# Kernel optimization log

Hardware: AMD Instinct MI355X
Metric: run time of the kernel (lower is better)

The kernel has to match this reference:

```python
import jax, jax.numpy as jnp
import numpy as np

N_NODES = 100000
N_EDGES = 1600000
IN_DIM = 48
HID = 16
N_CLASSES = 8


def _sage_conv(x, src, dst, W_l, W_r, b, n_nodes):
    # PyG SAGEConv (aggr='mean', root_weight=True):
    #   out_i = W_l @ mean_{j in N(i)} x_j + b + W_r @ x_i
    msg = x[src]                                              # [E, F]
    agg = jax.ops.segment_sum(msg, dst, num_segments=n_nodes)  # [N, F]
    deg = jax.ops.segment_sum(jnp.ones((src.shape[0],), x.dtype), dst,
                              num_segments=n_nodes)            # [N]
    agg = agg / jnp.maximum(deg, 1.0)[:, None]
    return agg @ W_l.T + b + x @ W_r.T


def setup_inputs() -> dict:
    key = jax.random.key(0)
    ks = jax.random.split(key, 10)
    def lin(k, out_d, in_d):
        s = 1.0 / np.sqrt(in_d)
        return jax.random.uniform(k, (out_d, in_d), jnp.float32, -s, s)
    x = jax.random.normal(ks[0], (N_NODES, IN_DIM), jnp.float32)
    edge_index = jax.random.randint(ks[1], (2, N_EDGES), 0, N_NODES, jnp.int64)
    return {
        "x": x,
        "edge_index": edge_index,
        "W1_l": lin(ks[2], HID, IN_DIM), "W1_r": lin(ks[3], HID, IN_DIM),
        "b1": jnp.zeros((HID,), jnp.float32),
        "W2_l": lin(ks[4], HID, HID), "W2_r": lin(ks[5], HID, HID),
        "b2": jnp.zeros((HID,), jnp.float32),
        "W3_l": lin(ks[6], N_CLASSES, HID), "W3_r": lin(ks[7], N_CLASSES, HID),
        "b3": jnp.zeros((N_CLASSES,), jnp.float32),
    }


def reference(x, edge_index, W1_l, W1_r, b1, W2_l, W2_r, b2, W3_l, W3_r, b3):
    src, dst = edge_index[0], edge_index[1]
    n = x.shape[0]
    # dropout is identity in deterministic/eval reference
    h = jax.nn.elu(_sage_conv(x, src, dst, W1_l, W1_r, b1, n))
    h = jax.nn.elu(_sage_conv(h, src, dst, W2_l, W2_r, b2, n))
    h = jax.nn.elu(_sage_conv(h, src, dst, W3_l, W3_r, b3, n))
    return jax.nn.log_softmax(h, axis=-1)
```

## Files before the change

kernel.cpp:

```cpp
#include <hip/hip_runtime.h>
#include <hip/hip_bf16.h>
#include <math.h>

#define N_IN   48
#define N_HID  16
#define N_CLS  8
#define CAP    48
#define NB_SHIFT 9
#define TILE   4096
#define CAPB   9216
#define WSTR   52

__device__ __forceinline__ float bf2f(unsigned short u) {
    union { unsigned int i; float f; } c;
    c.i = ((unsigned int)u) << 16;
    return c.f;
}
__device__ __forceinline__ unsigned short f2bf(float f) {
    unsigned int u = __float_as_uint(f);
    unsigned int r = u + 0x7FFFu + ((u >> 16) & 1u);
    return (unsigned short)(r >> 16);
}

__global__ __launch_bounds__(256) void proj48_kernel(
        const float* __restrict__ X,
        const float* __restrict__ Wl,
        const float* __restrict__ Wr,
        const float* __restrict__ b,
        unsigned short* __restrict__ P,
        float* __restrict__ S,
        int N) {
    __shared__ float sWl[N_HID * WSTR];
    __shared__ float sWr[N_HID * WSTR];
    __shared__ float sb[N_HID];
    int t = threadIdx.x;
    for (int idx = t; idx < N_HID * N_IN; idx += 256) {
        int r = idx / N_IN, k = idx - r * N_IN;
        sWl[r * WSTR + k] = Wl[idx];
        sWr[r * WSTR + k] = Wr[idx];
    }
    if (t < N_HID) sb[t] = b[t];
    __syncthreads();

    int node = blockIdx.x * 64 + (t >> 2);
    int q = t & 3;
    if (node >= N) return;

    const float4* xrow = reinterpret_cast<const float4*>(X + (size_t)node * N_IN);
    float accL[4], accR[4];
#pragma unroll
    for (int oo = 0; oo < 4; oo++) { accL[oo] = 0.0f; accR[oo] = sb[4 * q + oo]; }

#pragma unroll
    for (int c = 0; c < N_IN / 4; c++) {
        float4 xv = xrow[c];
#pragma unroll
        for (int oo = 0; oo < 4; oo++) {
            int row = 4 * q + oo;
            float4 wl = *reinterpret_cast<const float4*>(&sWl[row * WSTR + 4 * c]);
            float4 wr = *reinterpret_cast<const float4*>(&sWr[row * WSTR + 4 * c]);
            accL[oo] = fmaf(xv.x, wl.x, accL[oo]); accR[oo] = fmaf(xv.x, wr.x, accR[oo]);
            accL[oo] = fmaf(xv.y, wl.y, accL[oo]); accR[oo] = fmaf(xv.y, wr.y, accR[oo]);
            accL[oo] = fmaf(xv.z, wl.z, accL[oo]); accR[oo] = fmaf(xv.z, wr.z, accR[oo]);
            accL[oo] = fmaf(xv.w, wl.w, accL[oo]); accR[oo] = fmaf(xv.w, wr.w, accR[oo]);
        }
    }

    int gid = node * 4 + q;
    reinterpret_cast<ushort4*>(P)[gid] =
        make_ushort4(f2bf(accL[0]), f2bf(accL[1]), f2bf(accL[2]), f2bf(accL[3]));
    reinterpret_cast<float4*>(S)[gid] =
        make_float4(accR[0], accR[1], accR[2], accR[3]);
}

__global__ __launch_bounds__(256) void scatter_tiles_kernel(
        const int* __restrict__ src, const int* __restrict__ dst,
        int* __restrict__ cursor, int* __restrict__ ebuf, int E) {
    __shared__ int lh[256];
    __shared__ int gbase[256];
    __shared__ int rank[256];
    int t = threadIdx.x;
    lh[t] = 0;
    rank[t] = 0;
    __syncthreads();
    int base = blockIdx.x * TILE;
    int dcache[TILE / 256];
#pragma unroll
    for (int k = 0; k < TILE / 256; k++) {
        int e = base + t + k * 256;
        dcache[k] = -1;
        if (e < E) {
            int d = dst[e];
            dcache[k] = d;
            atomicAdd(&lh[d >> NB_SHIFT], 1);
        }
    }
    __syncthreads();
    if (lh[t]) gbase[t] = atomicAdd(&cursor[t], lh[t]);
    __syncthreads();
#pragma unroll
    for (int k = 0; k < TILE / 256; k++) {
        int e = base + t + k * 256;
        if (e < E) {
            int d = dcache[k];
            int b = d >> NB_SHIFT;
            int r = gbase[b] + atomicAdd(&rank[b], 1);
            if (r < CAPB)
                ebuf[b * CAPB + r] = ((d & 511) << 17) | src[e];
        }
    }
}

__global__ __launch_bounds__(256) void fine_fill_kernel(
        const int* __restrict__ cursor, const int* __restrict__ ebuf,
        int* __restrict__ cnt, int* __restrict__ adj, int N) {
    __shared__ int lc[512];
    int b = blockIdx.x;
    int nodeBeg = b << NB_SHIFT;
    for (int i = threadIdx.x; i < 512; i += 256) lc[i] = 0;
    __syncthreads();
    int beg = b * CAPB;
    int nb_cnt = cursor[b];
    if (nb_cnt > CAPB) nb_cnt = CAPB;
    int end = beg + nb_cnt;
    for (int e = beg + threadIdx.x; e < end; e += 256) {
        int v = ebuf[e];
        int ld = ((unsigned int)v) >> 17;
        int s  = v & 0x1FFFF;
        int p = atomicAdd(&lc[ld], 1);
        if (p < CAP) adj[(size_t)(nodeBeg + ld) * CAP + p] = s;
    }
    __syncthreads();
    for (int i = threadIdx.x; nodeBeg + i < N && i < 512; i += 256)
        cnt[nodeBeg + i] = lc[i];
}

__global__ __launch_bounds__(256) void gather_proj16_kernel(
        const int* __restrict__ cnt, const int* __restrict__ adj,
        const unsigned short* __restrict__ Pin, const float* __restrict__ Sin,
        const float* __restrict__ Wl, const float* __restrict__ Wr,
        const float* __restrict__ bias,
        unsigned short* __restrict__ Pout, float* __restrict__ Sout, int N) {
    int gid = blockIdx.x * blockDim.x + threadIdx.x;
    if (gid >= N * 4) return;
    int i = gid >> 2;
    int q = gid & 3;
    int deg = cnt[i];
    if (deg > CAP) deg = CAP;
    const int* lst = adj + (size_t)i * CAP;
    float4 sv = reinterpret_cast<const float4*>(Sin)[gid];
    float4 acc = make_float4(0.f, 0.f, 0.f, 0.f);
    const ushort4* P4 = reinterpret_cast<const ushort4*>(Pin);
    int e = 0;
    for (; e + 8 <= deg; e += 8) {
        int4 ja = *reinterpret_cast<const int4*>(lst + e);
        int4 jb = *reinterpret_cast<const int4*>(lst + e + 4);
        ushort4 t0 = P4[(size_t)ja.x * 4 + q];
        ushort4 t1 = P4[(size_t)ja.y * 4 + q];
        ushort4 t2 = P4[(size_t)ja.z * 4 + q];
        ushort4 t3 = P4[(size_t)ja.w * 4 + q];
        ushort4 t4 = P4[(size_t)jb.x * 4 + q];
        ushort4 t5 = P4[(size_t)jb.y * 4 + q];
        ushort4 t6 = P4[(size_t)jb.z * 4 + q];
        ushort4 t7 = P4[(size_t)jb.w * 4 + q];
        acc.x += ((bf2f(t0.x) + bf2f(t1.x)) + (bf2f(t2.x) + bf2f(t3.x)))
               + ((bf2f(t4.x) + bf2f(t5.x)) + (bf2f(t6.x) + bf2f(t7.x)));
        acc.y += ((bf2f(t0.y) + bf2f(t1.y)) + (bf2f(t2.y) + bf2f(t3.y)))
               + ((bf2f(t4.y) + bf2f(t5.y)) + (bf2f(t6.y) + bf2f(t7.y)));
        acc.z += ((bf2f(t0.z) + bf2f(t1.z)) + (bf2f(t2.z) + bf2f(t3.z)))
               + ((bf2f(t4.z) + bf2f(t5.z)) + (bf2f(t6.z) + bf2f(t7.z)));
        acc.w += ((bf2f(t0.w) + bf2f(t1.w)) + (bf2f(t2.w) + bf2f(t3.w)))
               + ((bf2f(t4.w) + bf2f(t5.w)) + (bf2f(t6.w) + bf2f(t7.w)));
    }
    for (; e + 4 <= deg; e += 4) {
        int4 js = *reinterpret_cast<const int4*>(lst + e);
        ushort4 t0 = P4[(size_t)js.x * 4 + q];
        ushort4 t1 = P4[(size_t)js.y * 4 + q];
        ushort4 t2 = P4[(size_t)js.z * 4 + q];
        ushort4 t3 = P4[(size_t)js.w * 4 + q];
        acc.x += (bf2f(t0.x) + bf2f(t1.x)) + (bf2f(t2.x) + bf2f(t3.x));
        acc.y += (bf2f(t0.y) + bf2f(t1.y)) + (bf2f(t2.y) + bf2f(t3.y));
        acc.z += (bf2f(t0.z) + bf2f(t1.z)) + (bf2f(t2.z) + bf2f(t3.z));
        acc.w += (bf2f(t0.w) + bf2f(t1.w)) + (bf2f(t2.w) + bf2f(t3.w));
    }
    for (; e < deg; e++) {
        ushort4 t = P4[(size_t)lst[e] * 4 + q];
        acc.x += bf2f(t.x); acc.y += bf2f(t.y);
        acc.z += bf2f(t.z); acc.w += bf2f(t.w);
    }
    float inv = 1.0f / (float)max(deg, 1);
    float4 h;
    h.x = acc.x * inv + sv.x; h.y = acc.y * inv + sv.y;
    h.z = acc.z * inv + sv.z; h.w = acc.w * inv + sv.w;
    h.x = h.x > 0.f ? h.x : expm1f(h.x);
    h.y = h.y > 0.f ? h.y : expm1f(h.y);
    h.z = h.z > 0.f ? h.z : expm1f(h.z);
    h.w = h.w > 0.f ? h.w : expm1f(h.w);

    int lane = threadIdx.x & 63;
    int lb = lane & ~3;
    float hv[16];
#pragma unroll
    for (int a = 0; a < 4; a++) {
        hv[4 * a + 0] = __shfl(h.x, lb + a, 64);
        hv[4 * a + 1] = __shfl(h.y, lb + a, 64);
        hv[4 * a + 2] = __shfl(h.z, lb + a, 64);
        hv[4 * a + 3] = __shfl(h.w, lb + a, 64);
    }

    const float4* Wl4 = reinterpret_cast<const float4*>(Wl);
    const float4* Wr4 = reinterpret_cast<const float4*>(Wr);
    float pl[4], sr[4];
#pragma unroll
    for (int oo = 0; oo < 4; oo++) {
        int o = 4 * q + oo;
        float aL = 0.0f, aR = bias[o];
#pragma unroll
        for (int c = 0; c < 4; c++) {
            float4 wl = Wl4[o * 4 + c];
            float4 wr = Wr4[o * 4 + c];
            aL = fmaf(hv[4 * c + 0], wl.x, aL); aR = fmaf(hv[4 * c + 0], wr.x, aR);
            aL = fmaf(hv[4 * c + 1], wl.y, aL); aR = fmaf(hv[4 * c + 1], wr.y, aR);
            aL = fmaf(hv[4 * c + 2], wl.z, aL); aR = fmaf(hv[4 * c + 2], wr.z, aR);
            aL = fmaf(hv[4 * c + 3], wl.w, aL); aR = fmaf(hv[4 * c + 3], wr.w, aR);
        }
        pl[oo] = aL; sr[oo] = aR;
    }
    reinterpret_cast<ushort4*>(Pout)[gid] =
        make_ushort4(f2bf(pl[0]), f2bf(pl[1]), f2bf(pl[2]), f2bf(pl[3]));
    reinterpret_cast<float4*>(Sout)[gid] = make_float4(sr[0], sr[1], sr[2], sr[3]);
}

__global__ __launch_bounds__(256) void gather_proj8_kernel(
        const int* __restrict__ cnt, const int* __restrict__ adj,
        const unsigned short* __restrict__ Pin, const float* __restrict__ Sin,
        const float* __restrict__ Wl, const float* __restrict__ Wr,
        const float* __restrict__ bias,
        unsigned short* __restrict__ Pout, float* __restrict__ Sout, int N) {
    int gid = blockIdx.x * blockDim.x + threadIdx.x;
    if (gid >= N * 4) return;
    int i = gid >> 2;
    int q = gid & 3;
    int deg = cnt[i];
    if (deg > CAP) deg = CAP;
    const int* lst = adj + (size_t)i * CAP;
    float4 sv = reinterpret_cast<const float4*>(Sin)[gid];
    float4 acc = make_float4(0.f, 0.f, 0.f, 0.f);
    const ushort4* P4 = reinterpret_cast<const ushort4*>(Pin);
    int e = 0;
    for (; e + 8 <= deg; e += 8) {
        int4 ja = *reinterpret_cast<const int4*>(lst + e);
        int4 jb = *reinterpret_cast<const int4*>(lst + e + 4);
        ushort4 t0 = P4[(size_t)ja.x * 4 + q];
        ushort4 t1 = P4[(size_t)ja.y * 4 + q];
        ushort4 t2 = P4[(size_t)ja.z * 4 + q];
        ushort4 t3 = P4[(size_t)ja.w * 4 + q];
        ushort4 t4 = P4[(size_t)jb.x * 4 + q];
        ushort4 t5 = P4[(size_t)jb.y * 4 + q];
        ushort4 t6 = P4[(size_t)jb.z * 4 + q];
        ushort4 t7 = P4[(size_t)jb.w * 4 + q];
        acc.x += ((bf2f(t0.x) + bf2f(t1.x)) + (bf2f(t2.x) + bf2f(t3.x)))
               + ((bf2f(t4.x) + bf2f(t5.x)) + (bf2f(t6.x) + bf2f(t7.x)));
        acc.y += ((bf2f(t0.y) + bf2f(t1.y)) + (bf2f(t2.y) + bf2f(t3.y)))
               + ((bf2f(t4.y) + bf2f(t5.y)) + (bf2f(t6.y) + bf2f(t7.y)));
        acc.z += ((bf2f(t0.z) + bf2f(t1.z)) + (bf2f(t2.z) + bf2f(t3.z)))
               + ((bf2f(t4.z) + bf2f(t5.z)) + (bf2f(t6.z) + bf2f(t7.z)));
        acc.w += ((bf2f(t0.w) + bf2f(t1.w)) + (bf2f(t2.w) + bf2f(t3.w)))
               + ((bf2f(t4.w) + bf2f(t5.w)) + (bf2f(t6.w) + bf2f(t7.w)));
    }
    for (; e + 4 <= deg; e += 4) {
        int4 js = *reinterpret_cast<const int4*>(lst + e);
        ushort4 t0 = P4[(size_t)js.x * 4 + q];
        ushort4 t1 = P4[(size_t)js.y * 4 + q];
        ushort4 t2 = P4[(size_t)js.z * 4 + q];
        ushort4 t3 = P4[(size_t)js.w * 4 + q];
        acc.x += (bf2f(t0.x) + bf2f(t1.x)) + (bf2f(t2.x) + bf2f(t3.x));
        acc.y += (bf2f(t0.y) + bf2f(t1.y)) + (bf2f(t2.y) + bf2f(t3.y));
        acc.z += (bf2f(t0.z) + bf2f(t1.z)) + (bf2f(t2.z) + bf2f(t3.z));
        acc.w += (bf2f(t0.w) + bf2f(t1.w)) + (bf2f(t2.w) + bf2f(t3.w));
    }
    for (; e < deg; e++) {
        ushort4 t = P4[(size_t)lst[e] * 4 + q];
        acc.x += bf2f(t.x); acc.y += bf2f(t.y);
        acc.z += bf2f(t.z); acc.w += bf2f(t.w);
    }
    float inv = 1.0f / (float)max(deg, 1);
    float4 h;
    h.x = acc.x * inv + sv.x; h.y = acc.y * inv + sv.y;
    h.z = acc.z * inv + sv.z; h.w = acc.w * inv + sv.w;
    h.x = h.x > 0.f ? h.x : expm1f(h.x);
    h.y = h.y > 0.f ? h.y : expm1f(h.y);
    h.z = h.z > 0.f ? h.z : expm1f(h.z);
    h.w = h.w > 0.f ? h.w : expm1f(h.w);

    int lane = threadIdx.x & 63;
    int lb = lane & ~3;
    float hv[16];
#pragma unroll
    for (int a = 0; a < 4; a++) {
        hv[4 * a + 0] = __shfl(h.x, lb + a, 64);
        hv[4 * a + 1] = __shfl(h.y, lb + a, 64);
        hv[4 * a + 2] = __shfl(h.z, lb + a, 64);
        hv[4 * a + 3] = __shfl(h.w, lb + a, 64);
    }

    const float4* Wl4 = reinterpret_cast<const float4*>(Wl);
    const float4* Wr4 = reinterpret_cast<const float4*>(Wr);
    float pl[2], sr[2];
#pragma unroll
    for (int oo = 0; oo < 2; oo++) {
        int o = 2 * q + oo;
        float aL = 0.0f, aR = bias[o];
#pragma unroll
        for (int c = 0; c < 4; c++) {
            float4 wl = Wl4[o * 4 + c];
            float4 wr = Wr4[o * 4 + c];
            aL = fmaf(hv[4 * c + 0], wl.x, aL); aR = fmaf(hv[4 * c + 0], wr.x, aR);
            aL = fmaf(hv[4 * c + 1], wl.y, aL); aR = fmaf(hv[4 * c + 1], wr.y, aR);
            aL = fmaf(hv[4 * c + 2], wl.z, aL); aR = fmaf(hv[4 * c + 2], wr.z, aR);
            aL = fmaf(hv[4 * c + 3], wl.w, aL); aR = fmaf(hv[4 * c + 3], wr.w, aR);
        }
        pl[oo] = aL; sr[oo] = aR;
    }
    unsigned int packed = ((unsigned int)f2bf(pl[1]) << 16) | f2bf(pl[0]);
    reinterpret_cast<unsigned int*>(Pout)[gid] = packed;
    reinterpret_cast<float2*>(Sout)[gid] = make_float2(sr[0], sr[1]);
}

__global__ __launch_bounds__(256) void gather8_kernel(
        const int* __restrict__ cnt, const int* __restrict__ adj,
        const unsigned short* __restrict__ P, const float* __restrict__ S,
        float* __restrict__ out, int N) {
    int gid = blockIdx.x * blockDim.x + threadIdx.x;
    if (gid >= N * 2) return;
    int i = gid >> 1;
    int q = gid & 1;
    int deg = cnt[i];
    if (deg > CAP) deg = CAP;
    const int* lst = adj + (size_t)i * CAP;
    float4 sv = reinterpret_cast<const float4*>(S)[gid];
    float4 acc = make_float4(0.f, 0.f, 0.f, 0.f);
    const ushort4* P4 = reinterpret_cast<const ushort4*>(P);
    int e = 0;
    for (; e + 8 <= deg; e += 8) {
        int4 ja = *reinterpret_cast<const int4*>(lst + e);
        int4 jb = *reinterpret_cast<const int4*>(lst + e + 4);
        ushort4 t0 = P4[(size_t)ja.x * 2 + q];
        ushort4 t1 = P4[(size_t)ja.y * 2 + q];
        ushort4 t2 = P4[(size_t)ja.z * 2 + q];
        ushort4 t3 = P4[(size_t)ja.w * 2 + q];
        ushort4 t4 = P4[(size_t)jb.x * 2 + q];
        ushort4 t5 = P4[(size_t)jb.y * 2 + q];
        ushort4 t6 = P4[(size_t)jb.z * 2 + q];
        ushort4 t7 = P4[(size_t)jb.w * 2 + q];
        acc.x += ((bf2f(t0.x) + bf2f(t1.x)) + (bf2f(t2.x) + bf2f(t3.x)))
               + ((bf2f(t4.x) + bf2f(t5.x)) + (bf2f(t6.x) + bf2f(t7.x)));
        acc.y += ((bf2f(t0.y) + bf2f(t1.y)) + (bf2f(t2.y) + bf2f(t3.y)))
               + ((bf2f(t4.y) + bf2f(t5.y)) + (bf2f(t6.y) + bf2f(t7.y)));
        acc.z += ((bf2f(t0.z) + bf2f(t1.z)) + (bf2f(t2.z) + bf2f(t3.z)))
               + ((bf2f(t4.z) + bf2f(t5.z)) + (bf2f(t6.z) + bf2f(t7.z)));
        acc.w += ((bf2f(t0.w) + bf2f(t1.w)) + (bf2f(t2.w) + bf2f(t3.w)))
               + ((bf2f(t4.w) + bf2f(t5.w)) + (bf2f(t6.w) + bf2f(t7.w)));
    }
    for (; e + 4 <= deg; e += 4) {
        int4 js = *reinterpret_cast<const int4*>(lst + e);
        ushort4 t0 = P4[(size_t)js.x * 2 + q];
        ushort4 t1 = P4[(size_t)js.y * 2 + q];
        ushort4 t2 = P4[(size_t)js.z * 2 + q];
        ushort4 t3 = P4[(size_t)js.w * 2 + q];
        acc.x += (bf2f(t0.x) + bf2f(t1.x)) + (bf2f(t2.x) + bf2f(t3.x));
        acc.y += (bf2f(t0.y) + bf2f(t1.y)) + (bf2f(t2.y) + bf2f(t3.y));
        acc.z += (bf2f(t0.z) + bf2f(t1.z)) + (bf2f(t2.z) + bf2f(t3.z));
        acc.w += (bf2f(t0.w) + bf2f(t1.w)) + (bf2f(t2.w) + bf2f(t3.w));
    }
    for (; e < deg; e++) {
        ushort4 t = P4[(size_t)lst[e] * 2 + q];
        acc.x += bf2f(t.x); acc.y += bf2f(t.y);
        acc.z += bf2f(t.z); acc.w += bf2f(t.w);
    }
    float inv = 1.0f / (float)max(deg, 1);
    float4 v;
    v.x = acc.x * inv + sv.x; v.y = acc.y * inv + sv.y;
    v.z = acc.z * inv + sv.z; v.w = acc.w * inv + sv.w;
    v.x = v.x > 0.f ? v.x : expm1f(v.x);
    v.y = v.y > 0.f ? v.y : expm1f(v.y);
    v.z = v.z > 0.f ? v.z : expm1f(v.z);
    v.w = v.w > 0.f ? v.w : expm1f(v.w);
    float m = fmaxf(fmaxf(v.x, v.y), fmaxf(v.z, v.w));
    m = fmaxf(m, __shfl_xor(m, 1));
    float sum = expf(v.x - m) + expf(v.y - m) + expf(v.z - m) + expf(v.w - m);
    sum += __shfl_xor(sum, 1);
    float lse = m + logf(sum);
    reinterpret_cast<float4*>(out)[gid] =
        make_float4(v.x - lse, v.y - lse, v.z - lse, v.w - lse);
}

extern "C" void kernel_launch(void* const* d_in, const int* in_sizes, int n_in,
                              void* d_out, int out_size, void* d_ws, size_t ws_size,
                              hipStream_t stream) {
    const float* x   = (const float*)d_in[0];
    const int*   ei  = (const int*)d_in[1];
    const float* W1l = (const float*)d_in[2];
    const float* W1r = (const float*)d_in[3];
    const float* b1  = (const float*)d_in[4];
    const float* W2l = (const float*)d_in[5];
    const float* W2r = (const float*)d_in[6];
    const float* b2  = (const float*)d_in[7];
    const float* W3l = (const float*)d_in[8];
    const float* W3r = (const float*)d_in[9];
    const float* b3  = (const float*)d_in[10];
    float* out = (float*)d_out;

    const int N = in_sizes[0] / N_IN;
    const int E = in_sizes[1] / 2;
    const int* src = ei;
    const int* dst = ei + E;
    const int nbuck = (N + 511) >> NB_SHIFT;

    int* cursor = (int*)d_ws;
    int* cnt    = cursor + 256;
    int  Npad   = (N + 3) & ~3;
    int* adj    = cnt + Npad;
    unsigned short* P1 = (unsigned short*)(adj + (size_t)N * CAP);
    unsigned short* P2 = P1 + (size_t)N * N_HID;
    float* S1 = (float*)(P2 + (size_t)N * N_HID);
    float* S3 = S1 + (size_t)N * N_HID;
    int* ebuf = (int*)P1;
    unsigned short* P3 = P1;

    hipMemsetAsync(cursor, 0, 256 * sizeof(int), stream);

    const int B = 256;
    int n4Grid   = (N * 4 + B - 1) / B;
    int n2Grid   = (N * 2 + B - 1) / B;
    int p1Grid   = (N + 63) / 64;
    int tileGrid = (E + TILE - 1) / TILE;

    scatter_tiles_kernel<<<tileGrid, B, 0, stream>>>(src, dst, cursor, ebuf, E);
    fine_fill_kernel<<<nbuck, B, 0, stream>>>(cursor, ebuf, cnt, adj, N);

    proj48_kernel<<<p1Grid, B, 0, stream>>>(x, W1l, W1r, b1, P1, S1, N);

    gather_proj16_kernel<<<n4Grid, B, 0, stream>>>(cnt, adj, P1, S1,
                                                   W2l, W2r, b2, P2, S1, N);

    gather_proj8_kernel<<<n4Grid, B, 0, stream>>>(cnt, adj, P2, S1,
                                                  W3l, W3r, b3, P3, S3, N);

    gather8_kernel<<<n2Grid, B, 0, stream>>>(cnt, adj, P3, S3, out, N);
}
```

Before: 231.9 us.

## Use compact per-bucket CSR adjacency and store root projections in bf16

Replaces the fixed-capacity padded adjacency (CAP=48 slots per node) with a compact per-bucket CSR layout. Each fine_fill block first counts degrees, runs a shared-memory prefix scan with 4-aligned row starts, then fills rows and publishes (rowstart, count) pairs. This cuts adjacency footprint and the cache lines touched during gathers, and removes the degree truncation at 48. Separately, the root-term S buffers are stored as bf16 instead of fp32 to halve their traffic. The costs are an extra pass over ebuf with more syncs in fine_fill, reduced precision for the self term, and possible overflow of the per-bucket capacity.

```diff
diff --git a/kernel.cpp b/kernel.cpp
--- a/kernel.cpp
+++ b/kernel.cpp
@@ -5,10 +5,10 @@
 #define N_IN   48
 #define N_HID  16
 #define N_CLS  8
-#define CAP    48
 #define NB_SHIFT 9
 #define TILE   4096
 #define CAPB   9216
+#define CAPB_ADJ 10752
 #define WSTR   52
 
 __device__ __forceinline__ float bf2f(unsigned short u) {
@@ -28,7 +28,7 @@
         const float* __restrict__ Wr,
         const float* __restrict__ b,
         unsigned short* __restrict__ P,
-        float* __restrict__ S,
+        unsigned short* __restrict__ S,
         int N) {
     __shared__ float sWl[N_HID * WSTR];
     __shared__ float sWr[N_HID * WSTR];
@@ -69,8 +69,8 @@
     int gid = node * 4 + q;
     reinterpret_cast<ushort4*>(P)[gid] =
         make_ushort4(f2bf(accL[0]), f2bf(accL[1]), f2bf(accL[2]), f2bf(accL[3]));
-    reinterpret_cast<float4*>(S)[gid] =
-        make_float4(accR[0], accR[1], accR[2], accR[3]);
+    reinterpret_cast<ushort4*>(S)[gid] =
+        make_ushort4(f2bf(accR[0]), f2bf(accR[1]), f2bf(accR[2]), f2bf(accR[3]));
 }
 
 __global__ __launch_bounds__(256) void scatter_tiles_kernel(
@@ -113,42 +113,72 @@
 
 __global__ __launch_bounds__(256) void fine_fill_kernel(
         const int* __restrict__ cursor, const int* __restrict__ ebuf,
-        int* __restrict__ cnt, int* __restrict__ adj, int N) {
+        int2* __restrict__ rs_cnt, int* __restrict__ adj, int N) {
     __shared__ int lc[512];
+    __shared__ int lr[512];
+    __shared__ int off[512];
+    __shared__ int psum[256];
     int b = blockIdx.x;
+    int t = threadIdx.x;
     int nodeBeg = b << NB_SHIFT;
-    for (int i = threadIdx.x; i < 512; i += 256) lc[i] = 0;
-    __syncthreads();
+    int adjBase = b * CAPB_ADJ;
+    lc[t] = 0; lc[t + 256] = 0;
+    lr[t] = 0; lr[t + 256] = 0;
+    __syncthreads();
+
     int beg = b * CAPB;
     int nb_cnt = cursor[b];
     if (nb_cnt > CAPB) nb_cnt = CAPB;
     int end = beg + nb_cnt;
-    for (int e = beg + threadIdx.x; e < end; e += 256) {
+    for (int e = beg + t; e < end; e += 256)
+        atomicAdd(&lc[((unsigned int)ebuf[e]) >> 17], 1);
+    __syncthreads();
+
+    int a0 = (lc[2 * t] + 3) & ~3;
+    int a1 = (lc[2 * t + 1] + 3) & ~3;
+    psum[t] = a0 + a1;
+    __syncthreads();
+#pragma unroll
+    for (int d = 1; d < 256; d <<= 1) {
+        int add = (t >= d) ? psum[t - d] : 0;
+        __syncthreads();
+        psum[t] += add;
+        __syncthreads();
+    }
+    int pairExcl = psum[t] - (a0 + a1);
+    off[2 * t] = pairExcl;
+    off[2 * t + 1] = pairExcl + a0;
+    __syncthreads();
+
+    for (int i = t; i < 512; i += 256) {
+        int node = nodeBeg + i;
+        if (node < N) rs_cnt[node] = make_int2(adjBase + off[i], lc[i]);
+    }
+
+    for (int e = beg + t; e < end; e += 256) {
         int v = ebuf[e];
         int ld = ((unsigned int)v) >> 17;
         int s  = v & 0x1FFFF;
-        int p = atomicAdd(&lc[ld], 1);
-        if (p < CAP) adj[(size_t)(nodeBeg + ld) * CAP + p] = s;
-    }
-    __syncthreads();
-    for (int i = threadIdx.x; nodeBeg + i < N && i < 512; i += 256)
-        cnt[nodeBeg + i] = lc[i];
+        int p = atomicAdd(&lr[ld], 1);
+        int idx = off[ld] + p;
+        if (idx < CAPB_ADJ) adj[adjBase + idx] = s;
+    }
 }
 
 __global__ __launch_bounds__(256) void gather_proj16_kernel(
-        const int* __restrict__ cnt, const int* __restrict__ adj,
-        const unsigned short* __restrict__ Pin, const float* __restrict__ Sin,
+        const int2* __restrict__ rs_cnt, const int* __restrict__ adj,
+        const unsigned short* __restrict__ Pin, const unsigned short* __restrict__ Sin,
         const float* __restrict__ Wl, const float* __restrict__ Wr,
         const float* __restrict__ bias,
-        unsigned short* __restrict__ Pout, float* __restrict__ Sout, int N) {
+        unsigned short* __restrict__ Pout, unsigned short* __restrict__ Sout, int N) {
     int gid = blockIdx.x * blockDim.x + threadIdx.x;
     if (gid >= N * 4) return;
     int i = gid >> 2;
     int q = gid & 3;
-    int deg = cnt[i];
-    if (deg > CAP) deg = CAP;
-    const int* lst = adj + (size_t)i * CAP;
-    float4 sv = reinterpret_cast<const float4*>(Sin)[gid];
+    int2 rc = rs_cnt[i];
+    int deg = rc.y;
+    const int* lst = adj + rc.x;
+    ushort4 svu = reinterpret_cast<const ushort4*>(Sin)[gid];
     float4 acc = make_float4(0.f, 0.f, 0.f, 0.f);
     const ushort4* P4 = reinterpret_cast<const ushort4*>(Pin);
     int e = 0;
@@ -190,8 +220,8 @@
     }
     float inv = 1.0f / (float)max(deg, 1);
     float4 h;
-    h.x = acc.x * inv + sv.x; h.y = acc.y * inv + sv.y;
-    h.z = acc.z * inv + sv.z; h.w = acc.w * inv + sv.w;
+    h.x = acc.x * inv + bf2f(svu.x); h.y = acc.y * inv + bf2f(svu.y);
+    h.z = acc.z * inv + bf2f(svu.z); h.w = acc.w * inv + bf2f(svu.w);
     h.x = h.x > 0.f ? h.x : expm1f(h.x);
     h.y = h.y > 0.f ? h.y : expm1f(h.y);
     h.z = h.z > 0.f ? h.z : expm1f(h.z);
@@ -228,23 +258,24 @@
     }
     reinterpret_cast<ushort4*>(Pout)[gid] =
         make_ushort4(f2bf(pl[0]), f2bf(pl[1]), f2bf(pl[2]), f2bf(pl[3]));
-    reinterpret_cast<float4*>(Sout)[gid] = make_float4(sr[0], sr[1], sr[2], sr[3]);
+    reinterpret_cast<ushort4*>(Sout)[gid] =
+        make_ushort4(f2bf(sr[0]), f2bf(sr[1]), f2bf(sr[2]), f2bf(sr[3]));
 }
 
 __global__ __launch_bounds__(256) void gather_proj8_kernel(
-        const int* __restrict__ cnt, const int* __restrict__ adj,
-        const unsigned short* __restrict__ Pin, const float* __restrict__ Sin,
+        const int2* __restrict__ rs_cnt, const int* __restrict__ adj,
+        const unsigned short* __restrict__ Pin, const unsigned short* __restrict__ Sin,
         const float* __restrict__ Wl, const float* __restrict__ Wr,
         const float* __restrict__ bias,
-        unsigned short* __restrict__ Pout, float* __restrict__ Sout, int N) {
+        unsigned short* __restrict__ Pout, unsigned short* __restrict__ Sout, int N) {
     int gid = blockIdx.x * blockDim.x + threadIdx.x;
     if (gid >= N * 4) return;
     int i = gid >> 2;
     int q = gid & 3;
-    int deg = cnt[i];
-    if (deg > CAP) deg = CAP;
-    const int* lst = adj + (size_t)i * CAP;
-    float4 sv = reinterpret_cast<const float4*>(Sin)[gid];
+    int2 rc = rs_cnt[i];
+    int deg = rc.y;
+    const int* lst = adj + rc.x;
+    ushort4 svu = reinterpret_cast<const ushort4*>(Sin)[gid];
     float4 acc = make_float4(0.f, 0.f, 0.f, 0.f);
     const ushort4* P4 = reinterpret_cast<const ushort4*>(Pin);
     int e = 0;
@@ -286,8 +317,8 @@
     }
     float inv = 1.0f / (float)max(deg, 1);
     float4 h;
-    h.x = acc.x * inv + sv.x; h.y = acc.y * inv + sv.y;
-    h.z = acc.z * inv + sv.z; h.w = acc.w * inv + sv.w;
+    h.x = acc.x * inv + bf2f(svu.x); h.y = acc.y * inv + bf2f(svu.y);
+    h.z = acc.z * inv + bf2f(svu.z); h.w = acc.w * inv + bf2f(svu.w);
     h.x = h.x > 0.f ? h.x : expm1f(h.x);
     h.y = h.y > 0.f ? h.y : expm1f(h.y);
     h.z = h.z > 0.f ? h.z : expm1f(h.z);
@@ -322,23 +353,24 @@
         }
         pl[oo] = aL; sr[oo] = aR;
     }
-    unsigned int packed = ((unsigned int)f2bf(pl[1]) << 16) | f2bf(pl[0]);
-    reinterpret_cast<unsigned int*>(Pout)[gid] = packed;
-    reinterpret_cast<float2*>(Sout)[gid] = make_float2(sr[0], sr[1]);
+    reinterpret_cast<unsigned int*>(Pout)[gid] =
+        ((unsigned int)f2bf(pl[1]) << 16) | f2bf(pl[0]);
+    reinterpret_cast<unsigned int*>(Sout)[gid] =
+        ((unsigned int)f2bf(sr[1]) << 16) | f2bf(sr[0]);
 }
 
 __global__ __launch_bounds__(256) void gather8_kernel(
-        const int* __restrict__ cnt, const int* __restrict__ adj,
-        const unsigned short* __restrict__ P, const float* __restrict__ S,
+        const int2* __restrict__ rs_cnt, const int* __restrict__ adj,
+        const unsigned short* __restrict__ P, const unsigned short* __restrict__ S,
         float* __restrict__ out, int N) {
     int gid = blockIdx.x * blockDim.x + threadIdx.x;
     if (gid >= N * 2) return;
     int i = gid >> 1;
     int q = gid & 1;
-    int deg = cnt[i];
-    if (deg > CAP) deg = CAP;
-    const int* lst = adj + (size_t)i * CAP;
-    float4 sv = reinterpret_cast<const float4*>(S)[gid];
+    int2 rc = rs_cnt[i];
+    int deg = rc.y;
+    const int* lst = adj + rc.x;
+    ushort4 svu = reinterpret_cast<const ushort4*>(S)[gid];
     float4 acc = make_float4(0.f, 0.f, 0.f, 0.f);
     const ushort4* P4 = reinterpret_cast<const ushort4*>(P);
     int e = 0;
@@ -380,8 +412,8 @@
     }
     float inv = 1.0f / (float)max(deg, 1);
     float4 v;
-    v.x = acc.x * inv + sv.x; v.y = acc.y * inv + sv.y;
-    v.z = acc.z * inv + sv.z; v.w = acc.w * inv + sv.w;
+    v.x = acc.x * inv + bf2f(svu.x); v.y = acc.y * inv + bf2f(svu.y);
+    v.z = acc.z * inv + bf2f(svu.z); v.w = acc.w * inv + bf2f(svu.w);
     v.x = v.x > 0.f ? v.x : expm1f(v.x);
     v.y = v.y > 0.f ? v.y : expm1f(v.y);
     v.z = v.z > 0.f ? v.z : expm1f(v.z);
@@ -417,14 +449,13 @@
     const int* dst = ei + E;
     const int nbuck = (N + 511) >> NB_SHIFT;
 
-    int* cursor = (int*)d_ws;
-    int* cnt    = cursor + 256;
-    int  Npad   = (N + 3) & ~3;
-    int* adj    = cnt + Npad;
-    unsigned short* P1 = (unsigned short*)(adj + (size_t)N * CAP);
+    int*  cursor = (int*)d_ws;
+    int2* rs_cnt = (int2*)(cursor + 256);
+    int*  adj    = (int*)(rs_cnt + N);
+    unsigned short* P1 = (unsigned short*)(adj + (size_t)nbuck * CAPB_ADJ);
     unsigned short* P2 = P1 + (size_t)N * N_HID;
-    float* S1 = (float*)(P2 + (size_t)N * N_HID);
-    float* S3 = S1 + (size_t)N * N_HID;
+    unsigned short* S1 = P2 + (size_t)N * N_HID;
+    unsigned short* S3 = S1 + (size_t)N * N_HID;
     int* ebuf = (int*)P1;
     unsigned short* P3 = P1;
 
@@ -437,15 +468,15 @@
     int tileGrid = (E + TILE - 1) / TILE;
 
     scatter_tiles_kernel<<<tileGrid, B, 0, stream>>>(src, dst, cursor, ebuf, E);
-    fine_fill_kernel<<<nbuck, B, 0, stream>>>(cursor, ebuf, cnt, adj, N);
+    fine_fill_kernel<<<nbuck, B, 0, stream>>>(cursor, ebuf, rs_cnt, adj, N);
 
     proj48_kernel<<<p1Grid, B, 0, stream>>>(x, W1l, W1r, b1, P1, S1, N);
 
-    gather_proj16_kernel<<<n4Grid, B, 0, stream>>>(cnt, adj, P1, S1,
+    gather_proj16_kernel<<<n4Grid, B, 0, stream>>>(rs_cnt, adj, P1, S1,
                                                    W2l, W2r, b2, P2, S1, N);
 
-    gather_proj8_kernel<<<n4Grid, B, 0, stream>>>(cnt, adj, P2, S1,
+    gather_proj8_kernel<<<n4Grid, B, 0, stream>>>(rs_cnt, adj, P2, S1,
                                                   W3l, W3r, b3, P3, S3, N);
 
-    gather8_kernel<<<n2Grid, B, 0, stream>>>(cnt, adj, P3, S3, out, N);
-}
+    gather8_kernel<<<n2Grid, B, 0, stream>>>(rs_cnt, adj, P3, S3, out, N);
+}
```

Result: no change. 232.8 us (+0.4%).

## Fuse adjacency fill with first-layer projection and store root terms in bf16

Applied to the files above, without the earlier changes.

Merges the bucket fill kernel and the 48-wide projection kernel into one launch, with block IDs split between the two roles so they run concurrently. The ebuf buffer moves to its own workspace region instead of aliasing P1, which that overlap requires. The root-weight terms S are now stored and read as bf16 rather than fp32, cutting their memory traffic in every gather layer at some cost in precision. The fused kernel reserves the weight shared memory even for fill blocks, which may lower occupancy.

```diff
diff --git a/kernel.cpp b/kernel.cpp
--- a/kernel.cpp
+++ b/kernel.cpp
@@ -20,57 +20,6 @@
     unsigned int u = __float_as_uint(f);
     unsigned int r = u + 0x7FFFu + ((u >> 16) & 1u);
     return (unsigned short)(r >> 16);
-}
-
-__global__ __launch_bounds__(256) void proj48_kernel(
-        const float* __restrict__ X,
-        const float* __restrict__ Wl,
-        const float* __restrict__ Wr,
-        const float* __restrict__ b,
-        unsigned short* __restrict__ P,
-        float* __restrict__ S,
-        int N) {
-    __shared__ float sWl[N_HID * WSTR];
-    __shared__ float sWr[N_HID * WSTR];
-    __shared__ float sb[N_HID];
-    int t = threadIdx.x;
-    for (int idx = t; idx < N_HID * N_IN; idx += 256) {
-        int r = idx / N_IN, k = idx - r * N_IN;
-        sWl[r * WSTR + k] = Wl[idx];
-        sWr[r * WSTR + k] = Wr[idx];
-    }
-    if (t < N_HID) sb[t] = b[t];
-    __syncthreads();
-
-    int node = blockIdx.x * 64 + (t >> 2);
-    int q = t & 3;
-    if (node >= N) return;
-
-    const float4* xrow = reinterpret_cast<const float4*>(X + (size_t)node * N_IN);
-    float accL[4], accR[4];
-#pragma unroll
-    for (int oo = 0; oo < 4; oo++) { accL[oo] = 0.0f; accR[oo] = sb[4 * q + oo]; }
-
-#pragma unroll
-    for (int c = 0; c < N_IN / 4; c++) {
-        float4 xv = xrow[c];
-#pragma unroll
-        for (int oo = 0; oo < 4; oo++) {
-            int row = 4 * q + oo;
-            float4 wl = *reinterpret_cast<const float4*>(&sWl[row * WSTR + 4 * c]);
-            float4 wr = *reinterpret_cast<const float4*>(&sWr[row * WSTR + 4 * c]);
-            accL[oo] = fmaf(xv.x, wl.x, accL[oo]); accR[oo] = fmaf(xv.x, wr.x, accR[oo]);
-            accL[oo] = fmaf(xv.y, wl.y, accL[oo]); accR[oo] = fmaf(xv.y, wr.y, accR[oo]);
-            accL[oo] = fmaf(xv.z, wl.z, accL[oo]); accR[oo] = fmaf(xv.z, wr.z, accR[oo]);
-            accL[oo] = fmaf(xv.w, wl.w, accL[oo]); accR[oo] = fmaf(xv.w, wr.w, accR[oo]);
-        }
-    }
-
-    int gid = node * 4 + q;
-    reinterpret_cast<ushort4*>(P)[gid] =
-        make_ushort4(f2bf(accL[0]), f2bf(accL[1]), f2bf(accL[2]), f2bf(accL[3]));
-    reinterpret_cast<float4*>(S)[gid] =
-        make_float4(accR[0], accR[1], accR[2], accR[3]);
 }
 
 __global__ __launch_bounds__(256) void scatter_tiles_kernel(
@@ -111,36 +60,86 @@
     }
 }
 
-__global__ __launch_bounds__(256) void fine_fill_kernel(
+__global__ __launch_bounds__(256) void fill_proj_kernel(
         const int* __restrict__ cursor, const int* __restrict__ ebuf,
-        int* __restrict__ cnt, int* __restrict__ adj, int N) {
-    __shared__ int lc[512];
-    int b = blockIdx.x;
-    int nodeBeg = b << NB_SHIFT;
-    for (int i = threadIdx.x; i < 512; i += 256) lc[i] = 0;
+        int* __restrict__ cnt, int* __restrict__ adj,
+        const float* __restrict__ X,
+        const float* __restrict__ Wl, const float* __restrict__ Wr,
+        const float* __restrict__ b,
+        unsigned short* __restrict__ P, unsigned short* __restrict__ S,
+        int N, int nbuck) {
+    __shared__ int   lc[512];
+    __shared__ float sWl[N_HID * WSTR];
+    __shared__ float sWr[N_HID * WSTR];
+    __shared__ float sb[N_HID];
+    int t = threadIdx.x;
+
+    if ((int)blockIdx.x < nbuck) {
+        int bb = blockIdx.x;
+        int nodeBeg = bb << NB_SHIFT;
+        for (int i = t; i < 512; i += 256) lc[i] = 0;
+        __syncthreads();
+        int nb = cursor[bb];
+        if (nb > CAPB) nb = CAPB;
+        int beg = bb * CAPB, end = beg + nb;
+        for (int e = beg + t; e < end; e += 256) {
+            int v = ebuf[e];
+            int ld = ((unsigned int)v) >> 17;
+            int s  = v & 0x1FFFF;
+            int p = atomicAdd(&lc[ld], 1);
+            if (p < CAP) adj[(size_t)(nodeBeg + ld) * CAP + p] = s;
+        }
+        __syncthreads();
+        for (int i = t; nodeBeg + i < N && i < 512; i += 256)
+            cnt[nodeBeg + i] = lc[i];
+        return;
+    }
+
+    for (int idx = t; idx < N_HID * N_IN; idx += 256) {
+        int r = idx / N_IN, k = idx - r * N_IN;
+        sWl[r * WSTR + k] = Wl[idx];
+        sWr[r * WSTR + k] = Wr[idx];
+    }
+    if (t < N_HID) sb[t] = b[t];
     __syncthreads();
-    int beg = b * CAPB;
-    int nb_cnt = cursor[b];
-    if (nb_cnt > CAPB) nb_cnt = CAPB;
-    int end = beg + nb_cnt;
-    for (int e = beg + threadIdx.x; e < end; e += 256) {
-        int v = ebuf[e];
-        int ld = ((unsigned int)v) >> 17;
-        int s  = v & 0x1FFFF;
-        int p = atomicAdd(&lc[ld], 1);
-        if (p < CAP) adj[(size_t)(nodeBeg + ld) * CAP + p] = s;
-    }
-    __syncthreads();
-    for (int i = threadIdx.x; nodeBeg + i < N && i < 512; i += 256)
-        cnt[nodeBeg + i] = lc[i];
+
+    int node = ((int)blockIdx.x - nbuck) * 64 + (t >> 2);
+    int q = t & 3;
+    if (node >= N) return;
+
+    const float4* xrow = reinterpret_cast<const float4*>(X + (size_t)node * N_IN);
+    float accL[4], accR[4];
+#pragma unroll
+    for (int oo = 0; oo < 4; oo++) { accL[oo] = 0.0f; accR[oo] = sb[4 * q + oo]; }
+
+#pragma unroll
+    for (int c = 0; c < N_IN / 4; c++) {
+        float4 xv = xrow[c];
+#pragma unroll
+        for (int oo = 0; oo < 4; oo++) {
+            int row = 4 * q + oo;
+            float4 wl = *reinterpret_cast<const float4*>(&sWl[row * WSTR + 4 * c]);
+            float4 wr = *reinterpret_cast<const float4*>(&sWr[row * WSTR + 4 * c]);
+            accL[oo] = fmaf(xv.x, wl.x, accL[oo]); accR[oo] = fmaf(xv.x, wr.x, accR[oo]);
+            accL[oo] = fmaf(xv.y, wl.y, accL[oo]); accR[oo] = fmaf(xv.y, wr.y, accR[oo]);
+            accL[oo] = fmaf(xv.z, wl.z, accL[oo]); accR[oo] = fmaf(xv.z, wr.z, accR[oo]);
+            accL[oo] = fmaf(xv.w, wl.w, accL[oo]); accR[oo] = fmaf(xv.w, wr.w, accR[oo]);
+        }
+    }
+
+    int gid = node * 4 + q;
+    reinterpret_cast<ushort4*>(P)[gid] =
+        make_ushort4(f2bf(accL[0]), f2bf(accL[1]), f2bf(accL[2]), f2bf(accL[3]));
+    reinterpret_cast<ushort4*>(S)[gid] =
+        make_ushort4(f2bf(accR[0]), f2bf(accR[1]), f2bf(accR[2]), f2bf(accR[3]));
 }
 
 __global__ __launch_bounds__(256) void gather_proj16_kernel(
         const int* __restrict__ cnt, const int* __restrict__ adj,
-        const unsigned short* __restrict__ Pin, const float* __restrict__ Sin,
+        const unsigned short* __restrict__ Pin, const unsigned short* __restrict__ Sin,
         const float* __restrict__ Wl, const float* __restrict__ Wr,
         const float* __restrict__ bias,
-        unsigned short* __restrict__ Pout, float* __restrict__ Sout, int N) {
+        unsigned short* __restrict__ Pout, unsigned short* __restrict__ Sout, int N) {
     int gid = blockIdx.x * blockDim.x + threadIdx.x;
     if (gid >= N * 4) return;
     int i = gid >> 2;
@@ -148,7 +147,7 @@
     int deg = cnt[i];
     if (deg > CAP) deg = CAP;
     const int* lst = adj + (size_t)i * CAP;
-    float4 sv = reinterpret_cast<const float4*>(Sin)[gid];
+    ushort4 svu = reinterpret_cast<const ushort4*>(Sin)[gid];
     float4 acc = make_float4(0.f, 0.f, 0.f, 0.f);
     const ushort4* P4 = reinterpret_cast<const ushort4*>(Pin);
     int e = 0;
@@ -190,8 +189,8 @@
     }
     float inv = 1.0f / (float)max(deg, 1);
     float4 h;
-    h.x = acc.x * inv + sv.x; h.y = acc.y * inv + sv.y;
-    h.z = acc.z * inv + sv.z; h.w = acc.w * inv + sv.w;
+    h.x = acc.x * inv + bf2f(svu.x); h.y = acc.y * inv + bf2f(svu.y);
+    h.z = acc.z * inv + bf2f(svu.z); h.w = acc.w * inv + bf2f(svu.w);
     h.x = h.x > 0.f ? h.x : expm1f(h.x);
     h.y = h.y > 0.f ? h.y : expm1f(h.y);
     h.z = h.z > 0.f ? h.z : expm1f(h.z);
@@ -228,15 +227,16 @@
     }
     reinterpret_cast<ushort4*>(Pout)[gid] =
         make_ushort4(f2bf(pl[0]), f2bf(pl[1]), f2bf(pl[2]), f2bf(pl[3]));
-    reinterpret_cast<float4*>(Sout)[gid] = make_float4(sr[0], sr[1], sr[2], sr[3]);
+    reinterpret_cast<ushort4*>(Sout)[gid] =
+        make_ushort4(f2bf(sr[0]), f2bf(sr[1]), f2bf(sr[2]), f2bf(sr[3]));
 }
 
 __global__ __launch_bounds__(256) void gather_proj8_kernel(
         const int* __restrict__ cnt, const int* __restrict__ adj,
-        const unsigned short* __restrict__ Pin, const float* __restrict__ Sin,
+        const unsigned short* __restrict__ Pin, const unsigned short* __restrict__ Sin,
         const float* __restrict__ Wl, const float* __restrict__ Wr,
         const float* __restrict__ bias,
-        unsigned short* __restrict__ Pout, float* __restrict__ Sout, int N) {
+        unsigned int* __restrict__ Pout, unsigned int* __restrict__ Sout, int N) {
     int gid = blockIdx.x * blockDim.x + threadIdx.x;
     if (gid >= N * 4) return;
     int i = gid >> 2;
@@ -244,7 +244,7 @@
     int deg = cnt[i];
     if (deg > CAP) deg = CAP;
     const int* lst = adj + (size_t)i * CAP;
-    float4 sv = reinterpret_cast<const float4*>(Sin)[gid];
+    ushort4 svu = reinterpret_cast<const ushort4*>(Sin)[gid];
     float4 acc = make_float4(0.f, 0.f, 0.f, 0.f);
     const ushort4* P4 = reinterpret_cast<const ushort4*>(Pin);
     int e = 0;
@@ -286,8 +286,8 @@
     }
     float inv = 1.0f / (float)max(deg, 1);
     float4 h;
-    h.x = acc.x * inv + sv.x; h.y = acc.y * inv + sv.y;
-    h.z = acc.z * inv + sv.z; h.w = acc.w * inv + sv.w;
+    h.x = acc.x * inv + bf2f(svu.x); h.y = acc.y * inv + bf2f(svu.y);
+    h.z = acc.z * inv + bf2f(svu.z); h.w = acc.w * inv + bf2f(svu.w);
     h.x = h.x > 0.f ? h.x : expm1f(h.x);
     h.y = h.y > 0.f ? h.y : expm1f(h.y);
     h.z = h.z > 0.f ? h.z : expm1f(h.z);
@@ -322,14 +322,13 @@
         }
         pl[oo] = aL; sr[oo] = aR;
     }
-    unsigned int packed = ((unsigned int)f2bf(pl[1]) << 16) | f2bf(pl[0]);
-    reinterpret_cast<unsigned int*>(Pout)[gid] = packed;
-    reinterpret_cast<float2*>(Sout)[gid] = make_float2(sr[0], sr[1]);
+    Pout[gid] = ((unsigned int)f2bf(pl[1]) << 16) | f2bf(pl[0]);
+    Sout[gid] = ((unsigned int)f2bf(sr[1]) << 16) | f2bf(sr[0]);
 }
 
 __global__ __launch_bounds__(256) void gather8_kernel(
         const int* __restrict__ cnt, const int* __restrict__ adj,
-        const unsigned short* __restrict__ P, const float* __restrict__ S,
+        const unsigned short* __restrict__ P, const unsigned short* __restrict__ S,
         float* __restrict__ out, int N) {
     int gid = blockIdx.x * blockDim.x + threadIdx.x;
     if (gid >= N * 2) return;
@@ -338,7 +337,7 @@
     int deg = cnt[i];
     if (deg > CAP) deg = CAP;
     const int* lst = adj + (size_t)i * CAP;
-    float4 sv = reinterpret_cast<const float4*>(S)[gid];
+    ushort4 svu = reinterpret_cast<const ushort4*>(S)[gid];
     float4 acc = make_float4(0.f, 0.f, 0.f, 0.f);
     const ushort4* P4 = reinterpret_cast<const ushort4*>(P);
     int e = 0;
@@ -380,8 +379,8 @@
     }
     float inv = 1.0f / (float)max(deg, 1);
     float4 v;
-    v.x = acc.x * inv + sv.x; v.y = acc.y * inv + sv.y;
-    v.z = acc.z * inv + sv.z; v.w = acc.w * inv + sv.w;
+    v.x = acc.x * inv + bf2f(svu.x); v.y = acc.y * inv + bf2f(svu.y);
+    v.z = acc.z * inv + bf2f(svu.z); v.w = acc.w * inv + bf2f(svu.w);
     v.x = v.x > 0.f ? v.x : expm1f(v.x);
     v.y = v.y > 0.f ? v.y : expm1f(v.y);
     v.z = v.z > 0.f ? v.z : expm1f(v.z);
@@ -421,11 +420,11 @@
     int* cnt    = cursor + 256;
     int  Npad   = (N + 3) & ~3;
     int* adj    = cnt + Npad;
-    unsigned short* P1 = (unsigned short*)(adj + (size_t)N * CAP);
+    int* ebuf   = adj + (size_t)N * CAP;
+    unsigned short* P1 = (unsigned short*)(ebuf + (size_t)nbuck * CAPB);
     unsigned short* P2 = P1 + (size_t)N * N_HID;
-    float* S1 = (float*)(P2 + (size_t)N * N_HID);
-    float* S3 = S1 + (size_t)N * N_HID;
-    int* ebuf = (int*)P1;
+    unsigned short* S1 = P2 + (size_t)N * N_HID;
+    unsigned short* S3 = S1 + (size_t)N * N_HID;
     unsigned short* P3 = P1;
 
     hipMemsetAsync(cursor, 0, 256 * sizeof(int), stream);
@@ -437,15 +436,17 @@
     int tileGrid = (E + TILE - 1) / TILE;
 
     scatter_tiles_kernel<<<tileGrid, B, 0, stream>>>(src, dst, cursor, ebuf, E);
-    fine_fill_kernel<<<nbuck, B, 0, stream>>>(cursor, ebuf, cnt, adj, N);
-
-    proj48_kernel<<<p1Grid, B, 0, stream>>>(x, W1l, W1r, b1, P1, S1, N);
+
+    fill_proj_kernel<<<nbuck + p1Grid, B, 0, stream>>>(
+        cursor, ebuf, cnt, adj, x, W1l, W1r, b1, P1, S1, N, nbuck);
 
     gather_proj16_kernel<<<n4Grid, B, 0, stream>>>(cnt, adj, P1, S1,
                                                    W2l, W2r, b2, P2, S1, N);
 
     gather_proj8_kernel<<<n4Grid, B, 0, stream>>>(cnt, adj, P2, S1,
-                                                  W3l, W3r, b3, P3, S3, N);
+                                                  W3l, W3r, b3,
+                                                  (unsigned int*)P3,
+                                                  (unsigned int*)S3, N);
 
     gather8_kernel<<<n2Grid, B, 0, stream>>>(cnt, adj, P3, S3, out, N);
 }
```

Result: faster. 218.6 us, median of 2 (-5.7%).
